# Performance work log

Measured on AMD Instinct MI355X. Metric: run time of the kernel, lower is better.

Reference implementation:

```python
import jax, jax.numpy as jnp
import numpy as np

N_VOX, N_CLUST, CLUST_SIZE, N_EDGE, N_FEAT = 200000, 2000, 100, 32000, 16


def setup_inputs() -> dict:
    key = jax.random.key(0)
    k1, k2, k3, k4 = jax.random.split(key, 4)
    data = jax.random.normal(k1, (N_VOX, 5), dtype=jnp.float32)
    clusts = jax.random.randint(k2, (N_CLUST, CLUST_SIZE), 0, N_VOX)
    edge_index = jax.random.randint(k3, (2, N_EDGE), 0, N_CLUST)
    W = jax.random.normal(k4, (5, N_FEAT), dtype=jnp.float32) * 0.1
    return {"data": data, "clusts": clusts, "edge_index": edge_index, "W": W}


def reference(data, clusts, edge_index, W):
    # Vectorized replacement of the per-edge Python loop:
    # gather all cluster voxels once, then gather per-edge endpoint clusters.
    cvox = data[clusts]                      # [C, V, 5]
    src = cvox[edge_index[0]]                # [E, V, 5]
    dst = cvox[edge_index[1]]                # [E, V, 5]
    cnn_data = jnp.concatenate([src, dst], axis=1)   # [E, 2V, 5]
    # overwrite batch-id column (index 3) with the edge id, as in the loop
    eids = jnp.arange(edge_index.shape[1], dtype=cnn_data.dtype)
    cnn_data = cnn_data.at[:, :, 3].set(eids[:, None])
    flat = cnn_data.reshape(-1, 5)           # [E*2V, 5]
    # stand-in for UResNet(...)['ppn_feature_dec'][0][0]: per-point feature map
    feats = jax.nn.relu(flat @ W)            # [E*2V, F]
    return feats
```

## Files before the change

### kernel.cpp

```cpp
#include <hip/hip_runtime.h>

#define N_VOX      200000
#define N_CLUST    2000
#define CLUST_SIZE 100
#define N_EDGE     32000
#define N_FEAT     16


#define TOTAL_QUADS (N_EDGE * 2 * CLUST_SIZE * 4)
#define HALF_QUADS  (TOTAL_QUADS / 2)
#define BLOCK       256
#define GRID        (HALF_QUADS / BLOCK)

typedef float f32x4 __attribute__((ext_vector_type(4)));

__global__ __launch_bounds__(BLOCK) void edge_enc_kernel(
    const float* __restrict__ data,
    const int*   __restrict__ clusts,
    const int*   __restrict__ edge_index,
    const float* __restrict__ W,
    float*       __restrict__ out)
{
    __shared__ float Ws[5 * N_FEAT];
    if (threadIdx.x < 5 * N_FEAT) {
        Ws[threadIdx.x] = W[threadIdx.x];
    }
    __syncthreads();

    const unsigned t = blockIdx.x * BLOCK + threadIdx.x;

    const unsigned fb    = t & 3u;
    const unsigned fbase = fb * 4u;

    float w0[4], w1[4], w2[4], w3[4], w4[4];
#pragma unroll
    for (int q = 0; q < 4; ++q) {
        w0[q] = Ws[0 * N_FEAT + fbase + q];
        w1[q] = Ws[1 * N_FEAT + fbase + q];
        w2[q] = Ws[2 * N_FEAT + fbase + q];
        w3[q] = Ws[3 * N_FEAT + fbase + q];
        w4[q] = Ws[4 * N_FEAT + fbase + q];
    }

    const unsigned g0 = t;
    const unsigned g1 = t + (unsigned)HALF_QUADS;

    const unsigned p0 = g0 >> 2;
    const unsigned p1 = g1 >> 2;

    const unsigned e0 = p0 / 200u;
    const unsigned e1 = p1 / 200u;
    const unsigned j0 = p0 - e0 * 200u;
    const unsigned j1 = p1 - e1 * 200u;
    const unsigned s0 = (j0 >= 100u) ? 1u : 0u;
    const unsigned s1 = (j1 >= 100u) ? 1u : 0u;
    const unsigned v0 = j0 - s0 * 100u;
    const unsigned v1 = j1 - s1 * 100u;

    const int c0 = edge_index[s0 * N_EDGE + e0];
    const int c1 = edge_index[s1 * N_EDGE + e1];

    const int vox0 = clusts[c0 * CLUST_SIZE + (int)v0];
    const int vox1 = clusts[c1 * CLUST_SIZE + (int)v1];

    const float* dr0 = data + (size_t)vox0 * 5;
    const float* dr1 = data + (size_t)vox1 * 5;
    const float a0 = dr0[0], a1 = dr0[1], a2 = dr0[2], a4 = dr0[4];
    const float b0 = dr1[0], b1 = dr1[1], b2 = dr1[2], b4 = dr1[4];
    const float a3 = (float)e0;
    const float b3 = (float)e1;

    float ra[4], rb[4];
#pragma unroll
    for (int q = 0; q < 4; ++q) {
        float va = fmaf(a0, w0[q], fmaf(a1, w1[q], fmaf(a2, w2[q],
                   fmaf(a3, w3[q], a4 * w4[q]))));
        float vb = fmaf(b0, w0[q], fmaf(b1, w1[q], fmaf(b2, w2[q],
                   fmaf(b3, w3[q], b4 * w4[q]))));
        ra[q] = fmaxf(va, 0.0f);
        rb[q] = fmaxf(vb, 0.0f);
    }

    f32x4 ova = { ra[0], ra[1], ra[2], ra[3] };
    f32x4 ovb = { rb[0], rb[1], rb[2], rb[3] };
    __builtin_nontemporal_store(ova,
        reinterpret_cast<f32x4*>(out + (size_t)p0 * N_FEAT + fbase));
    __builtin_nontemporal_store(ovb,
        reinterpret_cast<f32x4*>(out + (size_t)p1 * N_FEAT + fbase));
}

extern "C" void kernel_launch(void* const* d_in, const int* in_sizes, int n_in,
                              void* d_out, int out_size, void* d_ws, size_t ws_size,
                              hipStream_t stream) {
    const float* data       = (const float*)d_in[0];
    const int*   clusts     = (const int*)d_in[1];
    const int*   edge_index = (const int*)d_in[2];
    const float* W          = (const float*)d_in[3];
    float*       out        = (float*)d_out;

    edge_enc_kernel<<<GRID, BLOCK, 0, stream>>>(data, clusts, edge_index, W, out);
}
```

Measured before the change: 85.29 us.

## Precompute per-cluster-voxel partial features in workspace, then add edge-id term

Adds a precompute kernel that evaluates the linear projection of the four non-edge-id columns once per cluster voxel (200k points × 16 features) into the workspace buffer. The main kernel then gathers these 64-byte partial rows by cluster id, adds the edge-id times W row 3, and applies ReLU. This replaces the chained clusts→data gathers and five FMAs per output quad with a single 16-byte gather plus one FMA. The cost is an extra kernel launch and a 12.8 MB intermediate that has to be written and read back. The original direct kernel is kept as a fallback when the workspace is too small.

```diff
diff --git a/kernel.cpp b/kernel.cpp
--- a/kernel.cpp
+++ b/kernel.cpp
@@ -10,11 +10,92 @@
 #define TOTAL_QUADS (N_EDGE * 2 * CLUST_SIZE * 4)
 #define HALF_QUADS  (TOTAL_QUADS / 2)
 #define BLOCK       256
-#define GRID        (HALF_QUADS / BLOCK)
+#define GRID_MAIN   (HALF_QUADS / BLOCK)
+
+#define PRE_THREADS (N_CLUST * CLUST_SIZE * 4)
+#define GRID_PRE    (PRE_THREADS / BLOCK)
 
 typedef float f32x4 __attribute__((ext_vector_type(4)));
 
+__global__ __launch_bounds__(BLOCK) void precompute_kernel(
+    const float* __restrict__ data,
+    const int*   __restrict__ clusts,
+    const float* __restrict__ W,
+    float*       __restrict__ h)
+{
+    const unsigned t  = blockIdx.x * BLOCK + threadIdx.x;
+    const unsigned cv = t >> 2;
+    const unsigned fb = t & 3u;
+
+    const int vox = clusts[cv];
+
+    const f32x4* __restrict__ Wv = reinterpret_cast<const f32x4*>(W);
+    const f32x4 w0 = Wv[0 * 4 + fb];
+    const f32x4 w1 = Wv[1 * 4 + fb];
+    const f32x4 w2 = Wv[2 * 4 + fb];
+    const f32x4 w4 = Wv[4 * 4 + fb];
+
+    const float* dr = data + (size_t)vox * 5;
+    const float x0 = dr[0], x1 = dr[1], x2 = dr[2], x4 = dr[4];
+
+    f32x4 g;
+#pragma unroll
+    for (int q = 0; q < 4; ++q)
+        g[q] = fmaf(x0, w0[q], fmaf(x1, w1[q], fmaf(x2, w2[q], x4 * w4[q])));
+
+    *reinterpret_cast<f32x4*>(h + (size_t)cv * N_FEAT + fb * 4u) = g;
+}
+
 __global__ __launch_bounds__(BLOCK) void edge_enc_kernel(
+    const float* __restrict__ h,
+    const int*   __restrict__ edge_index,
+    const float* __restrict__ W,
+    float*       __restrict__ out)
+{
+    const unsigned t = blockIdx.x * BLOCK + threadIdx.x;
+
+    const unsigned fb    = t & 3u;
+    const unsigned fbase = fb * 4u;
+
+    const f32x4 w3 = reinterpret_cast<const f32x4*>(W)[3 * 4 + fb];
+
+    const unsigned p0 = t >> 2;
+    const unsigned p1 = (t + (unsigned)HALF_QUADS) >> 2;
+
+    const unsigned e0 = p0 / 200u;
+    const unsigned e1 = p1 / 200u;
+    const unsigned j0 = p0 - e0 * 200u;
+    const unsigned j1 = p1 - e1 * 200u;
+    const unsigned s0 = (j0 >= 100u) ? 1u : 0u;
+    const unsigned s1 = (j1 >= 100u) ? 1u : 0u;
+    const unsigned v0 = j0 - s0 * 100u;
+    const unsigned v1 = j1 - s1 * 100u;
+
+    const int c0 = edge_index[s0 * N_EDGE + e0];
+    const int c1 = edge_index[s1 * N_EDGE + e1];
+
+    const f32x4 h0 = *reinterpret_cast<const f32x4*>(
+        h + ((size_t)c0 * CLUST_SIZE + v0) * N_FEAT + fbase);
+    const f32x4 h1 = *reinterpret_cast<const f32x4*>(
+        h + ((size_t)c1 * CLUST_SIZE + v1) * N_FEAT + fbase);
+
+    const float fe0 = (float)e0;
+    const float fe1 = (float)e1;
+
+    f32x4 r0, r1;
+#pragma unroll
+    for (int q = 0; q < 4; ++q) {
+        r0[q] = fmaxf(fmaf(fe0, w3[q], h0[q]), 0.0f);
+        r1[q] = fmaxf(fmaf(fe1, w3[q], h1[q]), 0.0f);
+    }
+
+    __builtin_nontemporal_store(r0,
+        reinterpret_cast<f32x4*>(out + (size_t)p0 * N_FEAT + fbase));
+    __builtin_nontemporal_store(r1,
+        reinterpret_cast<f32x4*>(out + (size_t)p1 * N_FEAT + fbase));
+}
+
+__global__ __launch_bounds__(BLOCK) void edge_enc_direct_kernel(
     const float* __restrict__ data,
     const int*   __restrict__ clusts,
     const int*   __restrict__ edge_index,
@@ -22,13 +103,10 @@
     float*       __restrict__ out)
 {
     __shared__ float Ws[5 * N_FEAT];
-    if (threadIdx.x < 5 * N_FEAT) {
-        Ws[threadIdx.x] = W[threadIdx.x];
-    }
+    if (threadIdx.x < 5 * N_FEAT) Ws[threadIdx.x] = W[threadIdx.x];
     __syncthreads();
 
     const unsigned t = blockIdx.x * BLOCK + threadIdx.x;
-
     const unsigned fb    = t & 3u;
     const unsigned fbase = fb * 4u;
 
@@ -42,24 +120,15 @@
         w4[q] = Ws[4 * N_FEAT + fbase + q];
     }
 
-    const unsigned g0 = t;
-    const unsigned g1 = t + (unsigned)HALF_QUADS;
-
-    const unsigned p0 = g0 >> 2;
-    const unsigned p1 = g1 >> 2;
-
-    const unsigned e0 = p0 / 200u;
-    const unsigned e1 = p1 / 200u;
-    const unsigned j0 = p0 - e0 * 200u;
-    const unsigned j1 = p1 - e1 * 200u;
-    const unsigned s0 = (j0 >= 100u) ? 1u : 0u;
-    const unsigned s1 = (j1 >= 100u) ? 1u : 0u;
-    const unsigned v0 = j0 - s0 * 100u;
-    const unsigned v1 = j1 - s1 * 100u;
+    const unsigned p0 = t >> 2;
+    const unsigned p1 = (t + (unsigned)HALF_QUADS) >> 2;
+    const unsigned e0 = p0 / 200u, e1 = p1 / 200u;
+    const unsigned j0 = p0 - e0 * 200u, j1 = p1 - e1 * 200u;
+    const unsigned s0 = (j0 >= 100u) ? 1u : 0u, s1 = (j1 >= 100u) ? 1u : 0u;
+    const unsigned v0 = j0 - s0 * 100u, v1 = j1 - s1 * 100u;
 
     const int c0 = edge_index[s0 * N_EDGE + e0];
     const int c1 = edge_index[s1 * N_EDGE + e1];
-
     const int vox0 = clusts[c0 * CLUST_SIZE + (int)v0];
     const int vox1 = clusts[c1 * CLUST_SIZE + (int)v1];
 
@@ -67,22 +136,18 @@
     const float* dr1 = data + (size_t)vox1 * 5;
     const float a0 = dr0[0], a1 = dr0[1], a2 = dr0[2], a4 = dr0[4];
     const float b0 = dr1[0], b1 = dr1[1], b2 = dr1[2], b4 = dr1[4];
-    const float a3 = (float)e0;
-    const float b3 = (float)e1;
+    const float a3 = (float)e0, b3 = (float)e1;
 
-    float ra[4], rb[4];
+    f32x4 ova, ovb;
 #pragma unroll
     for (int q = 0; q < 4; ++q) {
         float va = fmaf(a0, w0[q], fmaf(a1, w1[q], fmaf(a2, w2[q],
                    fmaf(a3, w3[q], a4 * w4[q]))));
         float vb = fmaf(b0, w0[q], fmaf(b1, w1[q], fmaf(b2, w2[q],
                    fmaf(b3, w3[q], b4 * w4[q]))));
-        ra[q] = fmaxf(va, 0.0f);
-        rb[q] = fmaxf(vb, 0.0f);
+        ova[q] = fmaxf(va, 0.0f);
+        ovb[q] = fmaxf(vb, 0.0f);
     }
-
-    f32x4 ova = { ra[0], ra[1], ra[2], ra[3] };
-    f32x4 ovb = { rb[0], rb[1], rb[2], rb[3] };
     __builtin_nontemporal_store(ova,
         reinterpret_cast<f32x4*>(out + (size_t)p0 * N_FEAT + fbase));
     __builtin_nontemporal_store(ovb,
@@ -98,5 +163,13 @@
     const float* W          = (const float*)d_in[3];
     float*       out        = (float*)d_out;
 
-    edge_enc_kernel<<<GRID, BLOCK, 0, stream>>>(data, clusts, edge_index, W, out);
+    const size_t h_bytes = (size_t)N_CLUST * CLUST_SIZE * N_FEAT * sizeof(float);
+    if (ws_size >= h_bytes) {
+        float* h = (float*)d_ws;
+        precompute_kernel<<<GRID_PRE, BLOCK, 0, stream>>>(data, clusts, W, h);
+        edge_enc_kernel<<<GRID_MAIN, BLOCK, 0, stream>>>(h, edge_index, W, out);
+    } else {
+        edge_enc_direct_kernel<<<GRID_MAIN, BLOCK, 0, stream>>>(
+            data, clusts, edge_index, W, out);
+    }
 }
```

After: 113.1 us. +32.7%, slower.
